# Optimization experiments

Hardware: AMD Instinct MI355X
Metric: run time of the kernel (lower is better)

## Reference

```python
import jax, jax.numpy as jnp
import numpy as np

# Model dims (match init_kwargs)
D_MODEL = 2048
H = 16        # query heads
HKV = 4       # kv heads (GQA)
DS = 32       # semantic head dim (compressed)
DG = 32       # geometric head dim (compressed, RoPE'd)
DV = 64       # value head dim
B, T = 2, 4096
MB = 64       # mem_block
LW = 1024     # local_window
ROPE_BASE = 10000.0
NEG_INF = -1e9


def _rope(x, pos, base):
    # x: [B, h, T, d] with d even; standard rotate-half RoPE
    d = x.shape[-1]
    inv_freq = 1.0 / (base ** (jnp.arange(0, d, 2, dtype=jnp.float32) / d))
    ang = pos.astype(jnp.float32)[:, None] * inv_freq          # [T, d/2]
    cos, sin = jnp.cos(ang), jnp.sin(ang)                      # [T, d/2]
    x1, x2 = jnp.split(x, 2, axis=-1)
    return jnp.concatenate([x1 * cos - x2 * sin,
                            x2 * cos + x1 * sin], axis=-1)


def setup_inputs() -> dict:
    key = jax.random.key(0)
    ks = jax.random.split(key, 8)
    w = lambda k, sh: jax.random.normal(k, sh, jnp.float32) * 0.02
    return {
        "x": jax.random.normal(ks[0], (B, T, D_MODEL), jnp.float32),
        "Wq_sem": w(ks[1], (D_MODEL, H * DS)),
        "Wk_sem": w(ks[2], (D_MODEL, HKV * DS)),
        "Wq_geo": w(ks[3], (D_MODEL, H * DG)),
        "Wk_geo": w(ks[4], (D_MODEL, HKV * DG)),
        "Wv": w(ks[5], (D_MODEL, HKV * DV)),
        "Wo": w(ks[6], (H * DV, D_MODEL)),
        "logit_scale": jnp.zeros((H,), jnp.float32),
    }


def reference(x, Wq_sem, Wk_sem, Wq_geo, Wk_geo, Wv, Wo, logit_scale):
    Bq, Tq = x.shape[0], x.shape[1]
    split = lambda y, h, d: y.reshape(Bq, Tq, h, d).transpose(0, 2, 1, 3)
    # Decoupled projections
    q_sem = split(x @ Wq_sem, H, DS)      # [B,H,T,DS]
    k_sem = split(x @ Wk_sem, HKV, DS)    # [B,HKV,T,DS]
    q_geo = split(x @ Wq_geo, H, DG)
    k_geo = split(x @ Wk_geo, HKV, DG)
    v = split(x @ Wv, HKV, DV)            # [B,HKV,T,DV]
    pos = jnp.arange(Tq)
    # RoPE only on the geometric path
    q_geo = _rope(q_geo, pos, ROPE_BASE)
    k_geo = _rope(k_geo, pos, ROPE_BASE)
    # Memory-block summarization: mean-pool remote KV into one token per block
    remote = Tq - LW
    nblk = remote // MB
    pool = lambda a: jnp.concatenate(
        [a[:, :, :remote].reshape(Bq, HKV, nblk, MB, a.shape[-1]).mean(axis=3),
         a[:, :, remote:]], axis=2)
    k_sem2, k_geo2, v2 = pool(k_sem), pool(k_geo), pool(v)  # [B,HKV,K,*], K=nblk+LW
    k_pos = jnp.concatenate([jnp.arange(nblk) * MB + (MB - 1),
                             jnp.arange(remote, Tq)])        # [K]
    # GQA head-group broadcast
    rep = lambda a: jnp.repeat(a, H // HKV, axis=1)
    k_sem2, k_geo2, v2 = rep(k_sem2), rep(k_geo2), rep(v2)   # [B,H,K,*]
    # Decoupled scores: semantic + geometric, each with its own scale
    scores = (jnp.einsum('bhqd,bhkd->bhqk', q_sem, k_sem2) * (1.0 / jnp.sqrt(float(DS)))
              + jnp.einsum('bhqd,bhkd->bhqk', q_geo, k_geo2) * (1.0 / jnp.sqrt(float(DG))))
    # Learned per-head temperature
    scores = scores * jnp.exp(logit_scale)[None, :, None, None]
    # Causal mask over summarized key positions
    mask = k_pos[None, :] <= pos[:, None]                    # [T,K]
    scores = jnp.where(mask[None, None], scores, NEG_INF)
    probs = jax.nn.softmax(scores, axis=-1)
    out = jnp.einsum('bhqk,bhkd->bhqd', probs, v2)           # [B,H,T,DV]
    out = out.transpose(0, 2, 1, 3).reshape(Bq, Tq, H * DV)
    return out @ Wo                                          # [B,T,D_MODEL]
```

## Files before the change

kernel.cpp:

```cpp
#include <hip/hip_runtime.h>
#include <math.h>

#define B_  2
#define T_  4096
#define DM  2048
#define H_  16
#define HKV 4
#define DV_ 64
#define MB_ 64
#define LW_ 1024
#define REMOTE 3072
#define NBLK 48
#define KTOT 1072
#define NTILES 17

typedef __bf16 bf16x8 __attribute__((ext_vector_type(8)));
typedef float  f32x4  __attribute__((ext_vector_type(4)));

__device__ __forceinline__ float bf2f(unsigned short u) {
    unsigned int x = ((unsigned int)u) << 16;
    return __builtin_bit_cast(float, x);
}
__device__ __forceinline__ unsigned short f2bf(float f) {
    unsigned int x = __builtin_bit_cast(unsigned int, f);
    x = x + 0x7fffu + ((x >> 16) & 1u);
    return (unsigned short)(x >> 16);
}

__device__ __forceinline__ void gload16(const unsigned short* gsrc,
                                        unsigned short* ldst) {
    __builtin_amdgcn_global_load_lds(
        (const __attribute__((address_space(1))) void*)gsrc,
        (__attribute__((address_space(3))) void*)ldst,
        16, 0, 0);
}

__global__ void cvt_f32_to_bf16(const float* __restrict__ src,
                                unsigned short* __restrict__ dst, int n) {
    int i = (blockIdx.x * blockDim.x + threadIdx.x) * 4;
    if (i >= n) return;
    float4 v = *(const float4*)(src + i);
    ushort4 o;
    o.x = f2bf(v.x); o.y = f2bf(v.y); o.z = f2bf(v.z); o.w = f2bf(v.w);
    *(ushort4*)(dst + i) = o;
}

__global__ void transpose_cvt(const float* __restrict__ src,
                              unsigned short* __restrict__ dst, int R, int C) {
    __shared__ float tile[32][33];
    int ct = blockIdx.x, rt = blockIdx.y;
    int tx = threadIdx.x, ty = threadIdx.y;
    #pragma unroll
    for (int i = ty; i < 32; i += 8)
        tile[i][tx] = src[(size_t)(rt * 32 + i) * C + ct * 32 + tx];
    __syncthreads();
    #pragma unroll
    for (int i = ty; i < 32; i += 8)
        dst[(size_t)(ct * 32 + i) * R + rt * 32 + tx] = f2bf(tile[tx][i]);
}

template<int MODE>
__global__ __launch_bounds__(256, 3) void gemmP(
    const unsigned short* __restrict__ A,
    const unsigned short* __restrict__ BT,
    float* __restrict__ outF,
    unsigned short* __restrict__ qcat,
    unsigned short* __restrict__ kp,
    unsigned short* __restrict__ vt,
    int M, int N, int K, int nbx)
{
    extern __shared__ __align__(16) unsigned short lds[];

    const int tid = threadIdx.x;
    const int lane = tid & 63, w = tid >> 6;
    const int wr = w >> 1, wc = w & 1;
    const int l15 = lane & 15, lg = lane >> 4;

    const int cpx = gridDim.x >> 3;
    const int swz = (blockIdx.x & 7) * cpx + (blockIdx.x >> 3);
    const int bx = swz % nbx, by = swz / nbx;
    const int row0 = by * 128, col0 = bx * 128;

    const int scol = ((lane & 3) ^ ((lane >> 3) & 3)) * 8;
    const int srA = w * 16 + (lane >> 2);
    const unsigned short* Ag = A  + (size_t)row0 * K;
    const unsigned short* Bg = BT + (size_t)col0 * K;

    const int rdsw = (lg ^ ((l15 >> 1) & 3)) * 8;
    const int aoff = (wr * 64 + l15) * 32 + rdsw;
    const int boff = (wc * 64 + l15) * 32 + rdsw;

    const int NT = K >> 5;
    f32x4 acc[4][4] = {};

    auto stage = [&](int s, int kk) {
        unsigned short* sa = lds + s * 8192;
        unsigned short* sb = sa + 4096;
        #pragma unroll
        for (int j = 0; j < 2; j++) {
            gload16(Ag + (size_t)(srA + j * 64) * K + kk + scol,
                    sa + (j * 256 + w * 64) * 8);
            gload16(Bg + (size_t)(srA + j * 64) * K + kk + scol,
                    sb + (j * 256 + w * 64) * 8);
        }
    };

    stage(0, 0);
    stage(1, 32);
    asm volatile("s_waitcnt vmcnt(4)" ::: "memory");

    int rs = 0;
    for (int t = 0; t < NT; ++t) {
        __builtin_amdgcn_s_barrier();
        const bool st = (t + 2) < NT;
        if (st) stage(rs == 0 ? 2 : rs - 1, (t + 2) << 5);

        const unsigned short* As_ = lds + rs * 8192;
        const unsigned short* Bs_ = As_ + 4096;
        bf16x8 af[4], bfr[4];
        #pragma unroll
        for (int mf = 0; mf < 4; mf++)
            af[mf] = __builtin_bit_cast(bf16x8, *(const uint4*)&As_[aoff + mf * 512]);
        #pragma unroll
        for (int nf = 0; nf < 4; nf++)
            bfr[nf] = __builtin_bit_cast(bf16x8, *(const uint4*)&Bs_[boff + nf * 512]);

        __builtin_amdgcn_s_setprio(1);
        #pragma unroll
        for (int mf = 0; mf < 4; mf++)
            #pragma unroll
            for (int nf = 0; nf < 4; nf++)
                acc[mf][nf] = __builtin_amdgcn_mfma_f32_16x16x32_bf16(
                                  af[mf], bfr[nf], acc[mf][nf], 0, 0, 0);
        __builtin_amdgcn_s_setprio(0);

        if (st) asm volatile("s_waitcnt vmcnt(4)" ::: "memory");
        else    asm volatile("s_waitcnt vmcnt(0)" ::: "memory");
        rs = (rs == 2) ? 0 : rs + 1;
    }

    if (MODE == 1) {
        #pragma unroll
        for (int mf = 0; mf < 4; mf++)
            #pragma unroll
            for (int nf = 0; nf < 4; nf++)
                #pragma unroll
                for (int r = 0; r < 4; r++) {
                    int row = row0 + wr * 64 + mf * 16 + lg * 4 + r;
                    int col = col0 + wc * 64 + nf * 16 + l15;
                    outF[(size_t)row * N + col] = acc[mf][nf][r];
                }
    } else {
        const int cspan = col0 + wc * 64;
        const int tbase = row0 & 4095;
        const int bq = row0 >> 12;

        if ((cspan >= 512 && cspan < 1024) || (cspan >= 1152 && cspan < 1280)) {
            const float invf = exp2f(-(float)l15 * 0.8304820237218406f);
            #pragma unroll
            for (int mf = 0; mf < 4; mf++) {
                #pragma unroll
                for (int r = 0; r < 4; r++) {
                    float s, c;
                    sincosf((float)(tbase + wr*64 + mf*16 + lg*4 + r) * invf, &s, &c);
                    float a0 = acc[mf][0][r], a1 = acc[mf][1][r];
                    acc[mf][0][r] = a0 * c - a1 * s;
                    acc[mf][1][r] = a1 * c + a0 * s;
                    float a2 = acc[mf][2][r], a3 = acc[mf][3][r];
                    acc[mf][2][r] = a2 * c - a3 * s;
                    acc[mf][3][r] = a3 * c + a2 * s;
                }
            }
        }

        if (cspan < 1024) {
            #pragma unroll
            for (int nf = 0; nf < 4; nf++) {
                int col = cspan + nf * 16 + l15;
                int h = (col < 512) ? (col >> 5) : ((col - 512) >> 5);
                int d = (col < 512) ? (col & 31) : (32 + (col & 31));
                unsigned short* qb =
                    qcat + (((size_t)(bq * 16 + h)) * 4096 + tbase) * 64 + d;
                #pragma unroll
                for (int mf = 0; mf < 4; mf++)
                    #pragma unroll
                    for (int r = 0; r < 4; r++)
                        qb[(size_t)(wr*64 + mf*16 + lg*4 + r) * 64] =
                            f2bf(acc[mf][nf][r]);
            }
        } else if (tbase >= REMOTE) {
            #pragma unroll
            for (int nf = 0; nf < 4; nf++) {
                int col = cspan + nf * 16 + l15;
                #pragma unroll
                for (int mf = 0; mf < 4; mf++)
                    #pragma unroll
                    for (int r = 0; r < 4; r++) {
                        int key = tbase + wr*64 + mf*16 + lg*4 + r - 3024;
                        unsigned short hv = f2bf(acc[mf][nf][r]);
                        if (col < 1280) {
                            int g, dk;
                            if (col < 1152) { g = (col - 1024) >> 5; dk = col & 31; }
                            else            { g = (col - 1152) >> 5; dk = 32 + (col & 31); }
                            kp[(((size_t)(bq*4 + g)) * KTOT + key) * 64 + dk] = hv;
                        } else {
                            int g = (col - 1280) >> 6, dv = col & 63;
                            vt[(((size_t)(bq*4 + g)) * 64 + dv) * KTOT + key] = hv;
                        }
                    }
            }
        } else {
            #pragma unroll
            for (int nf = 0; nf < 4; nf++) {
                float ps = 0.f;
                #pragma unroll
                for (int mf = 0; mf < 4; mf++)
                    #pragma unroll
                    for (int r = 0; r < 4; r++) ps += acc[mf][nf][r];
                ps += __shfl_xor(ps, 16);
                ps += __shfl_xor(ps, 32);
                if (lane < 16) {
                    int col = cspan + nf * 16 + l15;
                    int key = (tbase >> 6) + wr;
                    unsigned short hv = f2bf(ps * (1.f / 64.f));
                    if (col < 1280) {
                        int g, dk;
                        if (col < 1152) { g = (col - 1024) >> 5; dk = col & 31; }
                        else            { g = (col - 1152) >> 5; dk = 32 + (col & 31); }
                        kp[(((size_t)(bq*4 + g)) * KTOT + key) * 64 + dk] = hv;
                    } else {
                        int g = (col - 1280) >> 6, dv = col & 63;
                        vt[(((size_t)(bq*4 + g)) * 64 + dv) * KTOT + key] = hv;
                    }
                }
            }
        }
    }
}

__global__ __launch_bounds__(256) void attn_fwd(
    const unsigned short* __restrict__ qcat,
    const unsigned short* __restrict__ kp,
    const unsigned short* __restrict__ vt,
    const float* __restrict__ ls,
    unsigned short* __restrict__ attn_out)
{
    __shared__ unsigned short Pl[4][32][72];

    const int tid = threadIdx.x;
    const int lane = tid & 63, w = tid >> 6;
    const int l15 = lane & 15, lg = lane >> 4;

    const int wid = blockIdx.x * 4 + w;
    const int hb = wid & 31;
    const int iu = wid >> 5;
    int i;
    if (iu < 32)       i = 127 - iu;
    else if (iu == 32) i = 0;
    else if (iu == 33) i = 1;
    else               i = iu - 32;
    const int h = hb & 15, b = hb >> 4, g = h >> 2;
    const int q0 = i * 32;

    int ktmax;
    if (q0 < 64) ktmax = NTILES;
    else {
        int lastkey = q0 + 31 - 3024;
        ktmax = (lastkey < NBLK) ? 1 : (lastkey / 64 + 1);
    }

    const float sc = __expf(ls[h]) * 0.17677669529663687f;

    bf16x8 aq[2][2];
    const unsigned short* qbase = qcat + (((size_t)(b * 16 + h)) * T_ + q0) * 64;
    #pragma unroll
    for (int rf = 0; rf < 2; rf++)
        #pragma unroll
        for (int kh = 0; kh < 2; kh++)
            aq[rf][kh] = __builtin_bit_cast(bf16x8,
                *(const uint4*)(qbase + (size_t)(rf*16 + l15)*64 + kh*32 + lg*8));

    float m[2][4], lrun[2][4];
    #pragma unroll
    for (int rf = 0; rf < 2; rf++)
        #pragma unroll
        for (int r = 0; r < 4; r++) { m[rf][r] = -1e9f; lrun[rf][r] = 0.f; }
    f32x4 oacc[2][4] = {};

    const unsigned short* kbase = kp + ((size_t)(b * 4 + g)) * KTOT * 64;
    const unsigned short* vbase = vt + ((size_t)(b * 4 + g)) * 64 * KTOT;

    for (int kt = 0; kt < ktmax; kt++) {
        const int kb = kt * 64;

        bf16x8 bk[4][2];
        #pragma unroll
        for (int nf = 0; nf < 4; nf++) {
            int krow = kb + nf*16 + l15;
            int krc = krow < KTOT ? krow : KTOT - 1;
            #pragma unroll
            for (int kh = 0; kh < 2; kh++)
                bk[nf][kh] = __builtin_bit_cast(bf16x8,
                    *(const uint4*)(kbase + (size_t)krc * 64 + kh*32 + lg*8));
        }

        f32x4 s[2][4] = {};
        #pragma unroll
        for (int rf = 0; rf < 2; rf++)
            #pragma unroll
            for (int nf = 0; nf < 4; nf++)
                #pragma unroll
                for (int kh = 0; kh < 2; kh++)
                    s[rf][nf] = __builtin_amdgcn_mfma_f32_16x16x32_bf16(
                                    aq[rf][kh], bk[nf][kh], s[rf][nf], 0, 0, 0);

        bf16x8 bv[4][2];
        #pragma unroll
        for (int nfv = 0; nfv < 4; nfv++)
            #pragma unroll
            for (int kh = 0; kh < 2; kh++) {
                int kc = kb + kh*32 + lg*8;
                int kcc = (kc + 8 <= KTOT) ? kc : KTOT - 8;
                bv[nfv][kh] = __builtin_bit_cast(bf16x8,
                    *(const uint4*)(vbase + (size_t)(nfv*16 + l15) * KTOT + kcc));
            }

        #pragma unroll
        for (int rf = 0; rf < 2; rf++) {
            #pragma unroll
            for (int r = 0; r < 4; r++) {
                const int qpos = q0 + rf*16 + lg*4 + r;
                float vals[4];
                float tmax = -INFINITY;
                #pragma unroll
                for (int nf = 0; nf < 4; nf++) {
                    int key = kb + nf*16 + l15;
                    float v = s[rf][nf][r] * sc;
                    int kpos = (key < NBLK) ? key * 64 + 63 : 3024 + key;
                    v = (key < KTOT) ? ((kpos <= qpos) ? v : -1e9f) : -INFINITY;
                    vals[nf] = v;
                    tmax = fmaxf(tmax, v);
                }
                #pragma unroll
                for (int d = 1; d < 16; d <<= 1)
                    tmax = fmaxf(tmax, __shfl_xor(tmax, d));
                float mn = fmaxf(m[rf][r], tmax);
                float scl = __expf(m[rf][r] - mn);
                m[rf][r] = mn;
                float rs = 0.f;
                #pragma unroll
                for (int nf = 0; nf < 4; nf++) {
                    unsigned short pb = f2bf(__expf(vals[nf] - mn));
                    rs += bf2f(pb);
                    Pl[w][rf*16 + lg*4 + r][nf*16 + l15] = pb;
                }
                #pragma unroll
                for (int d = 1; d < 16; d <<= 1)
                    rs += __shfl_xor(rs, d);
                lrun[rf][r] = lrun[rf][r] * scl + rs;
                #pragma unroll
                for (int nfv = 0; nfv < 4; nfv++)
                    oacc[rf][nfv][r] *= scl;
            }
        }

        #pragma unroll
        for (int rf = 0; rf < 2; rf++) {
            bf16x8 pa[2];
            #pragma unroll
            for (int kh = 0; kh < 2; kh++)
                pa[kh] = __builtin_bit_cast(bf16x8,
                    *(const uint4*)&Pl[w][rf*16 + l15][kh*32 + lg*8]);
            #pragma unroll
            for (int nfv = 0; nfv < 4; nfv++)
                #pragma unroll
                for (int kh = 0; kh < 2; kh++)
                    oacc[rf][nfv] = __builtin_amdgcn_mfma_f32_16x16x32_bf16(
                                        pa[kh], bv[nfv][kh], oacc[rf][nfv], 0, 0, 0);
        }
    }

    #pragma unroll
    for (int rf = 0; rf < 2; rf++) {
        #pragma unroll
        for (int r = 0; r < 4; r++) {
            float inv = 1.f / lrun[rf][r];
            int q = q0 + rf*16 + lg*4 + r;
            size_t obase = ((size_t)(b * T_ + q)) * 1024 + h * 64;
            #pragma unroll
            for (int nfv = 0; nfv < 4; nfv++)
                attn_out[obase + nfv*16 + l15] = f2bf(oacc[rf][nfv][r] * inv);
        }
    }
}

extern "C" void kernel_launch(void* const* d_in, const int* in_sizes, int n_in,
                              void* d_out, int out_size, void* d_ws, size_t ws_size,
                              hipStream_t stream) {
    const float* x      = (const float*)d_in[0];
    const float* Wq_sem = (const float*)d_in[1];
    const float* Wk_sem = (const float*)d_in[2];
    const float* Wq_geo = (const float*)d_in[3];
    const float* Wk_geo = (const float*)d_in[4];
    const float* Wv     = (const float*)d_in[5];
    const float* Wo     = (const float*)d_in[6];
    const float* ls     = (const float*)d_in[7];

    char* w = (char*)d_ws;
    auto alloc = [&](size_t bytes) {
        char* p = w;
        w += (bytes + 255) & ~(size_t)255;
        return p;
    };
    unsigned short* xb    = (unsigned short*)alloc((size_t)8192 * 2048 * 2);
    unsigned short* WcatT = (unsigned short*)alloc((size_t)1536 * 2048 * 2);
    unsigned short* WoT   = (unsigned short*)alloc((size_t)2048 * 1024 * 2);
    unsigned short* qcat  = (unsigned short*)alloc((size_t)2 * 16 * 4096 * 64 * 2);
    unsigned short* kp    = (unsigned short*)alloc((size_t)2 * 4 * 1072 * 64 * 2);
    unsigned short* vt    = (unsigned short*)alloc((size_t)2 * 4 * 1072 * 64 * 2);
    unsigned short* aout  = (unsigned short*)alloc((size_t)8192 * 1024 * 2);

    hipFuncSetAttribute(reinterpret_cast<const void*>(&gemmP<0>),
                        hipFuncAttributeMaxDynamicSharedMemorySize, 49152);
    hipFuncSetAttribute(reinterpret_cast<const void*>(&gemmP<1>),
                        hipFuncAttributeMaxDynamicSharedMemorySize, 49152);

    cvt_f32_to_bf16<<<16384, 256, 0, stream>>>(x, xb, 8192 * 2048);

    dim3 tb(32, 8);
    transpose_cvt<<<dim3(16, 64), tb, 0, stream>>>(Wq_sem, WcatT + (size_t)0    * 2048, 2048, 512);
    transpose_cvt<<<dim3(16, 64), tb, 0, stream>>>(Wq_geo, WcatT + (size_t)512  * 2048, 2048, 512);
    transpose_cvt<<<dim3( 4, 64), tb, 0, stream>>>(Wk_sem, WcatT + (size_t)1024 * 2048, 2048, 128);
    transpose_cvt<<<dim3( 4, 64), tb, 0, stream>>>(Wk_geo, WcatT + (size_t)1152 * 2048, 2048, 128);
    transpose_cvt<<<dim3( 8, 64), tb, 0, stream>>>(Wv,     WcatT + (size_t)1280 * 2048, 2048, 256);
    transpose_cvt<<<dim3(64, 32), tb, 0, stream>>>(Wo, WoT, 1024, 2048);

    gemmP<0><<<768, 256, 49152, stream>>>(
        xb, WcatT, nullptr, qcat, kp, vt, 8192, 1536, 2048, 12);

    attn_fwd<<<dim3(1024), 256, 0, stream>>>(qcat, kp, vt, ls, aout);

    gemmP<1><<<1024, 256, 49152, stream>>>(
        aout, WoT, (float*)d_out, nullptr, nullptr, nullptr, 8192, 2048, 1024, 16);
}
```

Baseline: 203.4 us.

## Enlarge GEMM tiles to 256x256 with 512 threads and 4-stage pipeline

Replaces the 128x128, 256-thread GEMM with a 256x256-tile, 512-thread kernel in which each warp computes 128x64. It uses a 4-slot LDS ring with loads issued three steps ahead, and splits the A and B staging around two MFMA halves. The aim is more data reuse per LDS load and better hiding of global-memory latency. The cost is much larger LDS use (128 KB), far fewer blocks (192/256), lower occupancy, and possible CU underuse for the projection GEMM.

```diff
diff --git a/kernel.cpp b/kernel.cpp
--- a/kernel.cpp
+++ b/kernel.cpp
@@ -60,7 +60,7 @@
 }
 
 template<int MODE>
-__global__ __launch_bounds__(256, 3) void gemmP(
+__global__ __launch_bounds__(512, 2) void gemm8p(
     const unsigned short* __restrict__ A,
     const unsigned short* __restrict__ BT,
     float* __restrict__ outF,
@@ -73,58 +73,60 @@
 
     const int tid = threadIdx.x;
     const int lane = tid & 63, w = tid >> 6;
-    const int wr = w >> 1, wc = w & 1;
+    const int wm = w >> 2, wn = w & 3;
     const int l15 = lane & 15, lg = lane >> 4;
 
     const int cpx = gridDim.x >> 3;
     const int swz = (blockIdx.x & 7) * cpx + (blockIdx.x >> 3);
     const int bx = swz % nbx, by = swz / nbx;
-    const int row0 = by * 128, col0 = bx * 128;
-
-    const int scol = ((lane & 3) ^ ((lane >> 3) & 3)) * 8;
-    const int srA = w * 16 + (lane >> 2);
+    const int row0 = by * 256, col0 = bx * 256;
+
     const unsigned short* Ag = A  + (size_t)row0 * K;
     const unsigned short* Bg = BT + (size_t)col0 * K;
 
-    const int rdsw = (lg ^ ((l15 >> 1) & 3)) * 8;
-    const int aoff = (wr * 64 + l15) * 32 + rdsw;
-    const int boff = (wc * 64 + l15) * 32 + rdsw;
+    const int sr0 = w * 16 + (lane >> 2);
+    const int sr1 = sr0 + 128;
+    const int sc0 = ((lane & 3) ^ ((sr0 >> 1) & 3)) << 3;
+
+    const int rdsw = (lg ^ ((l15 >> 1) & 3)) << 3;
+    const int aoff = (wm * 128 + l15) * 32 + rdsw;
+    const int boff = (wn * 64 + l15) * 32 + rdsw;
 
     const int NT = K >> 5;
-    f32x4 acc[4][4] = {};
-
-    auto stage = [&](int s, int kk) {
-        unsigned short* sa = lds + s * 8192;
-        unsigned short* sb = sa + 4096;
-        #pragma unroll
-        for (int j = 0; j < 2; j++) {
-            gload16(Ag + (size_t)(srA + j * 64) * K + kk + scol,
-                    sa + (j * 256 + w * 64) * 8);
-            gload16(Bg + (size_t)(srA + j * 64) * K + kk + scol,
-                    sb + (j * 256 + w * 64) * 8);
-        }
+    f32x4 acc[8][4] = {};
+
+    auto stageA = [&](int slot, int kk) {
+        unsigned short* sa = lds + slot * 16384;
+        gload16(Ag + (size_t)sr0 * K + kk + sc0, sa + w * 512);
+        gload16(Ag + (size_t)sr1 * K + kk + sc0, sa + 4096 + w * 512);
     };
-
-    stage(0, 0);
-    stage(1, 32);
-    asm volatile("s_waitcnt vmcnt(4)" ::: "memory");
-
-    int rs = 0;
+    auto stageB = [&](int slot, int kk) {
+        unsigned short* sb = lds + slot * 16384 + 8192;
+        gload16(Bg + (size_t)sr0 * K + kk + sc0, sb + w * 512);
+        gload16(Bg + (size_t)sr1 * K + kk + sc0, sb + 4096 + w * 512);
+    };
+
+    stageA(0, 0);  stageB(0, 0);
+    stageA(1, 32); stageB(1, 32);
+    stageA(2, 64); stageB(2, 64);
+    asm volatile("s_waitcnt vmcnt(8)" ::: "memory");
+
     for (int t = 0; t < NT; ++t) {
         __builtin_amdgcn_s_barrier();
-        const bool st = (t + 2) < NT;
-        if (st) stage(rs == 0 ? 2 : rs - 1, (t + 2) << 5);
-
-        const unsigned short* As_ = lds + rs * 8192;
-        const unsigned short* Bs_ = As_ + 4096;
-        bf16x8 af[4], bfr[4];
+        const unsigned short* As_ = lds + (t & 3) * 16384;
+        const unsigned short* Bs_ = As_ + 8192;
+        const int wslot = (t + 3) & 3;
+        const int kk3 = (t + 3) << 5;
+        const bool st = (t + 3) < NT;
+
+        if (st) stageA(wslot, kk3);
+        bf16x8 bfr[4], af[4];
+        #pragma unroll
+        for (int nf = 0; nf < 4; nf++)
+            bfr[nf] = __builtin_bit_cast(bf16x8, *(const uint4*)&Bs_[boff + nf * 512]);
         #pragma unroll
         for (int mf = 0; mf < 4; mf++)
             af[mf] = __builtin_bit_cast(bf16x8, *(const uint4*)&As_[aoff + mf * 512]);
-        #pragma unroll
-        for (int nf = 0; nf < 4; nf++)
-            bfr[nf] = __builtin_bit_cast(bf16x8, *(const uint4*)&Bs_[boff + nf * 512]);
-
         __builtin_amdgcn_s_setprio(1);
         #pragma unroll
         for (int mf = 0; mf < 4; mf++)
@@ -134,35 +136,50 @@
                                   af[mf], bfr[nf], acc[mf][nf], 0, 0, 0);
         __builtin_amdgcn_s_setprio(0);
 
-        if (st) asm volatile("s_waitcnt vmcnt(4)" ::: "memory");
-        else    asm volatile("s_waitcnt vmcnt(0)" ::: "memory");
-        rs = (rs == 2) ? 0 : rs + 1;
+        if (st) stageB(wslot, kk3);
+        bf16x8 af2[4];
+        #pragma unroll
+        for (int mf = 0; mf < 4; mf++)
+            af2[mf] = __builtin_bit_cast(bf16x8, *(const uint4*)&As_[aoff + (mf + 4) * 512]);
+        __builtin_amdgcn_s_setprio(1);
+        #pragma unroll
+        for (int mf = 0; mf < 4; mf++)
+            #pragma unroll
+            for (int nf = 0; nf < 4; nf++)
+                acc[mf + 4][nf] = __builtin_amdgcn_mfma_f32_16x16x32_bf16(
+                                      af2[mf], bfr[nf], acc[mf + 4][nf], 0, 0, 0);
+        __builtin_amdgcn_s_setprio(0);
+
+        if (t + 3 < NT)      asm volatile("s_waitcnt vmcnt(8)" ::: "memory");
+        else if (t + 2 < NT) asm volatile("s_waitcnt vmcnt(4)" ::: "memory");
+        else if (t + 1 < NT) asm volatile("s_waitcnt vmcnt(0)" ::: "memory");
     }
 
+    const int rbase = wm * 128;
     if (MODE == 1) {
         #pragma unroll
-        for (int mf = 0; mf < 4; mf++)
+        for (int mf = 0; mf < 8; mf++)
             #pragma unroll
             for (int nf = 0; nf < 4; nf++)
                 #pragma unroll
                 for (int r = 0; r < 4; r++) {
-                    int row = row0 + wr * 64 + mf * 16 + lg * 4 + r;
-                    int col = col0 + wc * 64 + nf * 16 + l15;
+                    int row = row0 + rbase + mf * 16 + lg * 4 + r;
+                    int col = col0 + wn * 64 + nf * 16 + l15;
                     outF[(size_t)row * N + col] = acc[mf][nf][r];
                 }
     } else {
-        const int cspan = col0 + wc * 64;
+        const int cspan = col0 + wn * 64;
         const int tbase = row0 & 4095;
         const int bq = row0 >> 12;
 
         if ((cspan >= 512 && cspan < 1024) || (cspan >= 1152 && cspan < 1280)) {
             const float invf = exp2f(-(float)l15 * 0.8304820237218406f);
             #pragma unroll
-            for (int mf = 0; mf < 4; mf++) {
+            for (int mf = 0; mf < 8; mf++) {
                 #pragma unroll
                 for (int r = 0; r < 4; r++) {
                     float s, c;
-                    sincosf((float)(tbase + wr*64 + mf*16 + lg*4 + r) * invf, &s, &c);
+                    sincosf((float)(tbase + rbase + mf*16 + lg*4 + r) * invf, &s, &c);
                     float a0 = acc[mf][0][r], a1 = acc[mf][1][r];
                     acc[mf][0][r] = a0 * c - a1 * s;
                     acc[mf][1][r] = a1 * c + a0 * s;
@@ -182,10 +199,10 @@
                 unsigned short* qb =
                     qcat + (((size_t)(bq * 16 + h)) * 4096 + tbase) * 64 + d;
                 #pragma unroll
-                for (int mf = 0; mf < 4; mf++)
+                for (int mf = 0; mf < 8; mf++)
                     #pragma unroll
                     for (int r = 0; r < 4; r++)
-                        qb[(size_t)(wr*64 + mf*16 + lg*4 + r) * 64] =
+                        qb[(size_t)(rbase + mf*16 + lg*4 + r) * 64] =
                             f2bf(acc[mf][nf][r]);
             }
         } else if (tbase >= REMOTE) {
@@ -193,10 +210,10 @@
             for (int nf = 0; nf < 4; nf++) {
                 int col = cspan + nf * 16 + l15;
                 #pragma unroll
-                for (int mf = 0; mf < 4; mf++)
+                for (int mf = 0; mf < 8; mf++)
                     #pragma unroll
                     for (int r = 0; r < 4; r++) {
-                        int key = tbase + wr*64 + mf*16 + lg*4 + r - 3024;
+                        int key = tbase + rbase + mf*16 + lg*4 + r - 3024;
                         unsigned short hv = f2bf(acc[mf][nf][r]);
                         if (col < 1280) {
                             int g, dk;
@@ -211,26 +228,29 @@
             }
         } else {
             #pragma unroll
-            for (int nf = 0; nf < 4; nf++) {
-                float ps = 0.f;
-                #pragma unroll
-                for (int mf = 0; mf < 4; mf++)
+            for (int half = 0; half < 2; half++) {
+                #pragma unroll
+                for (int nf = 0; nf < 4; nf++) {
+                    float ps = 0.f;
                     #pragma unroll
-                    for (int r = 0; r < 4; r++) ps += acc[mf][nf][r];
-                ps += __shfl_xor(ps, 16);
-                ps += __shfl_xor(ps, 32);
-                if (lane < 16) {
-                    int col = cspan + nf * 16 + l15;
-                    int key = (tbase >> 6) + wr;
-                    unsigned short hv = f2bf(ps * (1.f / 64.f));
-                    if (col < 1280) {
-                        int g, dk;
-                        if (col < 1152) { g = (col - 1024) >> 5; dk = col & 31; }
-                        else            { g = (col - 1152) >> 5; dk = 32 + (col & 31); }
-                        kp[(((size_t)(bq*4 + g)) * KTOT + key) * 64 + dk] = hv;
-                    } else {
-                        int g = (col - 1280) >> 6, dv = col & 63;
-                        vt[(((size_t)(bq*4 + g)) * 64 + dv) * KTOT + key] = hv;
+                    for (int mf = half * 4; mf < half * 4 + 4; mf++)
+                        #pragma unroll
+                        for (int r = 0; r < 4; r++) ps += acc[mf][nf][r];
+                    ps += __shfl_xor(ps, 16);
+                    ps += __shfl_xor(ps, 32);
+                    if (lane < 16) {
+                        int col = cspan + nf * 16 + l15;
+                        int key = ((tbase + rbase) >> 6) + half;
+                        unsigned short hv = f2bf(ps * (1.f / 64.f));
+                        if (col < 1280) {
+                            int g, dk;
+                            if (col < 1152) { g = (col - 1024) >> 5; dk = col & 31; }
+                            else            { g = (col - 1152) >> 5; dk = 32 + (col & 31); }
+                            kp[(((size_t)(bq*4 + g)) * KTOT + key) * 64 + dk] = hv;
+                        } else {
+                            int g = (col - 1280) >> 6, dv = col & 63;
+                            vt[(((size_t)(bq*4 + g)) * 64 + dv) * KTOT + key] = hv;
+                        }
                     }
                 }
             }
@@ -420,10 +440,10 @@
     unsigned short* vt    = (unsigned short*)alloc((size_t)2 * 4 * 1072 * 64 * 2);
     unsigned short* aout  = (unsigned short*)alloc((size_t)8192 * 1024 * 2);
 
-    hipFuncSetAttribute(reinterpret_cast<const void*>(&gemmP<0>),
-                        hipFuncAttributeMaxDynamicSharedMemorySize, 49152);
-    hipFuncSetAttribute(reinterpret_cast<const void*>(&gemmP<1>),
-                        hipFuncAttributeMaxDynamicSharedMemorySize, 49152);
+    hipFuncSetAttribute(reinterpret_cast<const void*>(&gemm8p<0>),
+                        hipFuncAttributeMaxDynamicSharedMemorySize, 131072);
+    hipFuncSetAttribute(reinterpret_cast<const void*>(&gemm8p<1>),
+                        hipFuncAttributeMaxDynamicSharedMemorySize, 131072);
 
     cvt_f32_to_bf16<<<16384, 256, 0, stream>>>(x, xb, 8192 * 2048);
 
@@ -435,11 +455,11 @@
     transpose_cvt<<<dim3( 8, 64), tb, 0, stream>>>(Wv,     WcatT + (size_t)1280 * 2048, 2048, 256);
     transpose_cvt<<<dim3(64, 32), tb, 0, stream>>>(Wo, WoT, 1024, 2048);
 
-    gemmP<0><<<768, 256, 49152, stream>>>(
-        xb, WcatT, nullptr, qcat, kp, vt, 8192, 1536, 2048, 12);
+    gemm8p<0><<<192, 512, 131072, stream>>>(
+        xb, WcatT, nullptr, qcat, kp, vt, 8192, 1536, 2048, 6);
 
     attn_fwd<<<dim3(1024), 256, 0, stream>>>(qcat, kp, vt, ls, aout);
 
-    gemmP<1><<<1024, 256, 49152, stream>>>(
-        aout, WoT, (float*)d_out, nullptr, nullptr, nullptr, 8192, 2048, 1024, 16);
-}
+    gemm8p<1><<<256, 512, 131072, stream>>>(
+        aout, WoT, (float*)d_out, nullptr, nullptr, nullptr, 8192, 2048, 1024, 8);
+}
```

Result: slower. 214.4 us (+5.4%).
